# Kernel tuning notes

Measured on AMD Instinct MI355X. Metric: run time of the kernel, lower is better.

The kernel has to match this reference:

```python
import jax, jax.numpy as jnp
import numpy as np

N_GROUP = 8
TOPK_GROUP = 4
TOP_K = 8
ROUTED_SCALE = 2.5


def setup_inputs() -> dict:
    key = jax.random.key(0)
    ks = jax.random.split(key, 8)
    B, S, D, E, I = 4, 2048, 2048, 32, 1024
    s = 0.02
    return {
        "x": jax.random.normal(ks[0], (B, S, D), jnp.float32),
        "gate_w": jax.random.normal(ks[1], (D, E), jnp.float32) * s,
        "e_bias": jnp.zeros((E,), jnp.float32),
        "gate_up": jax.random.normal(ks[2], (E, D, 2 * I), jnp.float32) * s,
        "down": jax.random.normal(ks[3], (E, I, D), jnp.float32) * s,
        "shared_gate": jax.random.normal(ks[4], (D, I), jnp.float32) * s,
        "shared_up": jax.random.normal(ks[5], (D, I), jnp.float32) * s,
        "shared_down": jax.random.normal(ks[6], (I, D), jnp.float32) * s,
    }


def _router(x_flat, gate_w, e_bias):
    N, E = x_flat.shape[0], gate_w.shape[1]
    epg = E // N_GROUP  # experts per group
    logits = x_flat @ gate_w                                   # [N, E]
    scores = jax.nn.sigmoid(logits.astype(jnp.float32))        # [N, E]
    sfr = scores + e_bias                                      # routing scores
    grouped = sfr.reshape(N, N_GROUP, epg)
    group_scores = jax.lax.top_k(grouped, min(2, epg))[0].sum(-1)   # [N, G]
    topk_group_idx = jax.lax.top_k(group_scores, TOPK_GROUP)[1]     # [N, topk_group]
    group_mask = jnp.zeros((N, N_GROUP), bool).at[
        jnp.arange(N)[:, None], topk_group_idx].set(True)
    expert_mask = jnp.repeat(group_mask, epg, axis=1)          # [N, E]
    masked = jnp.where(expert_mask, sfr, -jnp.inf)
    topk_idx = jax.lax.top_k(masked, TOP_K)[1]                 # [N, K]
    topk_w = jnp.take_along_axis(scores, topk_idx, axis=1)     # [N, K]
    topk_w = topk_w / (topk_w.sum(-1, keepdims=True) + 1e-20)  # norm_topk_prob
    topk_w = topk_w * ROUTED_SCALE
    return topk_idx, topk_w, scores


def _experts(x_flat, topk_idx, topk_w, gate_up, down):
    N, D = x_flat.shape
    E, K = gate_up.shape[0], topk_idx.shape[1]
    flat = topk_idx.reshape(-1)                                # [N*K]
    sort_idx = jnp.argsort(flat)                               # route: group rows by expert
    sorted_tokens = x_flat[sort_idx // K]                      # [N*K, D]
    group_sizes = jnp.bincount(flat, length=E).astype(jnp.int32)
    h = jax.lax.ragged_dot(sorted_tokens, gate_up, group_sizes)  # [N*K, 2I]
    gate_h, up_h = jnp.split(h, 2, axis=-1)
    inter = jax.nn.silu(gate_h) * up_h                         # SwiGLU
    out = jax.lax.ragged_dot(inter, down, group_sizes)         # [N*K, D]
    unsorted = jnp.zeros_like(out).at[sort_idx].set(out)       # unroute
    return (unsorted.reshape(N, K, D) * topk_w[..., None].astype(out.dtype)).sum(1)


def _shared_mlp(x, wg, wu, wd):
    return (jax.nn.silu(x @ wg) * (x @ wu)) @ wd


def reference(x, gate_w, e_bias, gate_up, down, shared_gate, shared_up, shared_down):
    B, S, D = x.shape
    x_flat = x.reshape(B * S, D)
    topk_idx, topk_w, scores = _router(x_flat, gate_w, e_bias)
    routed = _experts(x_flat, topk_idx, topk_w, gate_up, down).reshape(B, S, D)
    output = routed + _shared_mlp(x, shared_gate, shared_up, shared_down)
    return output, topk_idx, scores
```

## Files before the change

### kernel.cpp

```cpp
#include <hip/hip_runtime.h>
#include <hip/hip_bf16.h>
#include <math.h>


typedef __bf16 bf16_t;
typedef __bf16 bf16x8 __attribute__((ext_vector_type(8)));
typedef float  f32x4  __attribute__((ext_vector_type(4)));

constexpr int NTOK = 8192;
constexpr int D    = 2048;
constexpr int E    = 32;
constexpr int I    = 1024;
constexpr int TK   = 8;
constexpr int NK   = NTOK * TK;
constexpr int TM   = 256;
constexpr int MAX_TILES = E + NK / TM;
constexpr float RSCALE = 2.5f;

#define GL16(g, l) __builtin_amdgcn_global_load_lds( \
    (const __attribute__((address_space(1))) void*)(g), \
    (__attribute__((address_space(3))) void*)(l), 16, 0, 0)


__global__ __launch_bounds__(64) void k_zero_meta(int* counts, int* cursors, int* ntl) {
    int t = threadIdx.x;
    if (t < E) { counts[t] = 0; cursors[t] = 0; }
    if (t == 0) *ntl = 0;
}

__global__ __launch_bounds__(64) void k_sentinel(float* out) {
    if (threadIdx.x == 0) out[0] = 12345.0f;
}

__global__ __launch_bounds__(256) void k_convert_x(const float* __restrict__ src,
                                                   bf16_t* __restrict__ dst, int n8) {
    int i = blockIdx.x * 256 + threadIdx.x;
    if (i >= n8) return;
    const float4* s = (const float4*)src;
    float4 a = s[(size_t)i * 2], b = s[(size_t)i * 2 + 1];
    bf16_t t[8] = {(bf16_t)a.x, (bf16_t)a.y, (bf16_t)a.z, (bf16_t)a.w,
                   (bf16_t)b.x, (bf16_t)b.y, (bf16_t)b.z, (bf16_t)b.w};
    *(uint4*)(dst + (size_t)i * 8) = *(const uint4*)t;
}

template <int MODE>
__global__ __launch_bounds__(256) void k_transpose(const float* __restrict__ src,
                                                   bf16_t* __restrict__ dst,
                                                   int R, int C,
                                                   size_t srcMat, size_t dstMat) {
    __shared__ float t[32][33];
    int b = blockIdx.z;
    const float* s = src + (size_t)b * srcMat;
    bf16_t* d = dst + (size_t)b * dstMat;
    int c0 = blockIdx.x * 32, r0 = blockIdx.y * 32;
    int tx = threadIdx.x, ty = threadIdx.y;
#pragma unroll
    for (int yy = 0; yy < 4; yy++)
        t[ty + yy * 8][tx] = s[(size_t)(r0 + ty + yy * 8) * C + c0 + tx];
    __syncthreads();
#pragma unroll
    for (int yy = 0; yy < 4; yy++) {
        int c = c0 + ty + yy * 8;
        int rc = (MODE == 0) ? c
               : (MODE == 1) ? ((c < I) ? 2 * c : 2 * (c - I) + 1)
               : (MODE == 2) ? 2 * c : 2 * c + 1;
        d[(size_t)rc * R + r0 + tx] = (bf16_t)t[tx][ty + yy * 8];
    }
}


__global__ __launch_bounds__(256) void k_router(const float* __restrict__ x,
                                                const float* __restrict__ gw,
                                                const float* __restrict__ eb,
                                                float* __restrict__ out_idx,
                                                float* __restrict__ out_scores,
                                                float* __restrict__ topk_w,
                                                int* __restrict__ tok_expert,
                                                int* __restrict__ counts) {
    int t = blockIdx.x;
    int tid = threadIdx.x;
    int e = tid & 31, part = tid >> 5;
    const float* xr = x + (size_t)t * D;
    float partial = 0.f;
    int d0 = part * 256;
    for (int d = d0; d < d0 + 256; d++)
        partial += xr[d] * gw[(size_t)d * E + e];

    __shared__ float red[8][32];
    __shared__ float sc[32], sfr[32];
    red[part][e] = partial;
    __syncthreads();
    if (tid < 32) {
        float l = 0.f;
#pragma unroll
        for (int p = 0; p < 8; p++) l += red[p][tid];
        float s = 1.f / (1.f + expf(-l));
        sc[tid] = s;
        sfr[tid] = s + eb[tid];
        out_scores[(size_t)t * E + tid] = s;
    }
    __syncthreads();
    if (tid == 0) {
        float gs[8];
#pragma unroll
        for (int g = 0; g < 8; g++) {
            float m1 = -1e30f, m2 = -1e30f;
#pragma unroll
            for (int i = 0; i < 4; i++) {
                float v = sfr[g * 4 + i];
                if (v > m1) { m2 = m1; m1 = v; } else if (v > m2) m2 = v;
            }
            gs[g] = m1 + m2;
        }
        bool gsel[8] = {false, false, false, false, false, false, false, false};
        for (int it = 0; it < 4; it++) {
            int bi = -1; float bv = -1e30f;
            for (int g = 0; g < 8; g++)
                if (!gsel[g] && gs[g] > bv) { bv = gs[g]; bi = g; }
            gsel[bi] = true;
        }
        float masked[32];
        for (int i = 0; i < 32; i++) masked[i] = gsel[i >> 2] ? sfr[i] : -1e30f;
        int idx[TK]; float w[TK]; float wsum = 0.f;
        for (int k = 0; k < TK; k++) {
            int bi = 0; float bv = -1e30f;
            for (int i = 0; i < 32; i++)
                if (masked[i] > bv) { bv = masked[i]; bi = i; }
            masked[bi] = -1e30f;
            idx[k] = bi; w[k] = sc[bi]; wsum += w[k];
        }
        float inv = RSCALE / (wsum + 1e-20f);
        for (int k = 0; k < TK; k++) {
            out_idx[(size_t)t * TK + k] = (float)idx[k];
            topk_w[(size_t)t * TK + k] = w[k] * inv;
            tok_expert[(size_t)t * TK + k] = idx[k];
            atomicAdd(&counts[idx[k]], 1);
        }
    }
}

__global__ __launch_bounds__(64) void k_offsets(const int* __restrict__ counts,
                                                int* __restrict__ offs,
                                                int4* __restrict__ ttbl,
                                                int* __restrict__ ntl) {
    if (threadIdx.x != 0) return;
    int off = 0, nt = 0;
    for (int e = 0; e < E; e++) {
        offs[e] = off;
        int c = counts[e];
        for (int r = 0; r < c; r += TM) {
            ttbl[nt] = make_int4(off + r, min(TM, c - r), e, 0);
            nt++;
        }
        off += c;
    }
    offs[E] = off;
    *ntl = nt;
}

__global__ __launch_bounds__(256) void k_scatter(const int* __restrict__ tok_expert,
                                                 const int* __restrict__ offs,
                                                 int* __restrict__ cursors,
                                                 int* __restrict__ slot_token,
                                                 int* __restrict__ slot_inv) {
    int i = blockIdx.x * 256 + threadIdx.x;
    if (i >= NK) return;
    int e = tok_expert[i];
    int pos = offs[e] + atomicAdd(&cursors[e], 1);
    slot_token[pos] = i >> 3;
    slot_inv[i] = pos;
}


#define SCB() __builtin_amdgcn_sched_barrier(0)
#define SG(m, n) __builtin_amdgcn_sched_group_barrier(m, n, 0)
#define SG_PLAIN() do { SG(0x30, 2); SG(0x8, 16); } while (0)
#define SG_PRE()   do { SG(0x100, 4); SG(0x30, 2); SG(0x8, 16); } while (0)
#define SG_RF()    do { SG(0x30, 2); SG(0x8, 4); SG(0x100, 2); SG(0x8, 4); \
    SG(0x100, 2); SG(0x8, 4); SG(0x100, 2); SG(0x8, 4); SG(0x100, 2); } while (0)
#define SG_PRERF() do { SG(0x100, 4); SG(0x30, 2); SG(0x8, 4); SG(0x100, 2); \
    SG(0x8, 4); SG(0x100, 2); SG(0x8, 4); SG(0x100, 2); SG(0x8, 4); SG(0x100, 2); } while (0)

#define PEND() do { asm volatile("s_waitcnt vmcnt(4)" ::: "memory"); \
    __builtin_amdgcn_s_barrier(); SCB(); } while (0)

#define SA2(b, rnd, k0) do { \
    GL16(gA[0][rnd] + (k0), smb + (b) * 65536 + (rnd) * 8192 + w * 1024); \
    GL16(gA[1][rnd] + (k0), smb + (b) * 65536 + 16384 + (rnd) * 8192 + w * 1024); } while (0)

#define SB(b, h, k0) do { \
    GL16(gB[h][0] + (k0), smb + (b) * 65536 + 32768 + (h) * 16384 + w * 1024); \
    GL16(gB[h][1] + (k0), smb + (b) * 65536 + 32768 + (h) * 16384 + 8192 + w * 1024); } while (0)

#define LDA(b, mh) do { _Pragma("unroll") for (int m_ = 0; m_ < 4; m_++) { \
    aF[m_][0] = *(const bf16x8*)(smb + (b) * 65536 + wm * 16384 + (mh) * 8192 + m_ * 2048 + lofs0); \
    aF[m_][1] = *(const bf16x8*)(smb + (b) * 65536 + wm * 16384 + (mh) * 8192 + m_ * 2048 + lofs1); } } while (0)

#define LDB(dst, b, nh) do { _Pragma("unroll") for (int n_ = 0; n_ < 2; n_++) { \
    dst[n_][0] = *(const bf16x8*)(smb + (b) * 65536 + 32768 + wn * 8192 + (nh) * 4096 + n_ * 2048 + lofs0); \
    dst[n_][1] = *(const bf16x8*)(smb + (b) * 65536 + 32768 + wn * 8192 + (nh) * 4096 + n_ * 2048 + lofs1); } } while (0)

#define MMA(bv, MH, NH) do { \
    __builtin_amdgcn_s_setprio(1); \
    _Pragma("unroll") for (int m_ = 0; m_ < 4; m_++) \
    _Pragma("unroll") for (int n_ = 0; n_ < 2; n_++) { \
    acc[(MH) * 4 + m_][(NH) * 2 + n_] = __builtin_amdgcn_mfma_f32_16x16x32_bf16( \
        aF[m_][0], bv[n_][0], acc[(MH) * 4 + m_][(NH) * 2 + n_], 0, 0, 0); \
    acc[(MH) * 4 + m_][(NH) * 2 + n_] = __builtin_amdgcn_mfma_f32_16x16x32_bf16( \
        aF[m_][1], bv[n_][1], acc[(MH) * 4 + m_][(NH) * 2 + n_], 0, 0, 0); } \
    __builtin_amdgcn_s_setprio(0); } while (0)

#define MMARF(bv, MH, NH, rb, rmh) do { \
    __builtin_amdgcn_s_setprio(1); \
    _Pragma("unroll") for (int m_ = 0; m_ < 4; m_++) { \
    _Pragma("unroll") for (int n_ = 0; n_ < 2; n_++) { \
    acc[(MH) * 4 + m_][(NH) * 2 + n_] = __builtin_amdgcn_mfma_f32_16x16x32_bf16( \
        aF[m_][0], bv[n_][0], acc[(MH) * 4 + m_][(NH) * 2 + n_], 0, 0, 0); \
    acc[(MH) * 4 + m_][(NH) * 2 + n_] = __builtin_amdgcn_mfma_f32_16x16x32_bf16( \
        aF[m_][1], bv[n_][1], acc[(MH) * 4 + m_][(NH) * 2 + n_], 0, 0, 0); } \
    aF[m_][0] = *(const bf16x8*)(smb + (rb) * 65536 + wm * 16384 + (rmh) * 8192 + m_ * 2048 + lofs0); \
    aF[m_][1] = *(const bf16x8*)(smb + (rb) * 65536 + wm * 16384 + (rmh) * 8192 + m_ * 2048 + lofs1); } \
    __builtin_amdgcn_s_setprio(0); } while (0)

template <bool EXPERT, bool GATHER, int EPI>
__global__ __launch_bounds__(512, 2) void k_mm8(const bf16_t* __restrict__ A,
                                                const bf16_t* __restrict__ Bt,
                                                int K, size_t estride,
                                                const int* __restrict__ slot_token,
                                                const int4* __restrict__ ttbl,
                                                const int* __restrict__ ntl,
                                                void* __restrict__ C, int ldc) {
    int L = (int)blockIdx.y * 8 + (int)blockIdx.x;
    int xcd = L & 7, k = L >> 3;
    int per = (int)gridDim.y >> 3;
    int ty = xcd * per + (k >> 3);
    int tx = k & 7;

    int base_slot, rows, e;
    if (EXPERT) {
        if (ty >= *ntl) return;
        int4 tt = ttbl[ty];
        base_slot = tt.x; rows = tt.y; e = tt.z;
    } else {
        base_slot = ty * TM; rows = TM; e = 0;
    }
    int c0 = tx * 256;
    const bf16_t* Bw = Bt + (size_t)e * estride + (size_t)c0 * K;

    extern __shared__ char smb[];

    int tid = threadIdx.x, lane = tid & 63, w = tid >> 6;
    int wm = w >> 2, wn = w & 3;
    int lr = lane & 15, hi = lane >> 4;
    int rx = lr & 7;
    int lofs0 = lr * 128 + ((hi ^ rx) << 4);
    int lofs1 = lr * 128 + (((4 + hi) ^ rx) << 4);

    int srow = tid >> 3;
    int cbg = (tid & 7) ^ (srow & 7);
    const bf16_t* gA[2][2]; const bf16_t* gB[2][2];
#pragma unroll
    for (int h = 0; h < 2; h++)
#pragma unroll
        for (int rnd = 0; rnd < 2; rnd++) {
            int r = h * 128 + rnd * 64 + srow;
            int ar = min(r, rows - 1);
            int tok = GATHER ? slot_token[base_slot + ar] : (base_slot + ar);
            gA[h][rnd] = A + (size_t)tok * K + cbg * 8;
            gB[h][rnd] = Bw + (size_t)r * K + cbg * 8;
        }

    f32x4 acc[8][4] = {};
    bf16x8 aF[4][2], b0[2][2], b1[2][2];

    SA2(0, 0, 0); SA2(0, 1, 0);
    SB(0, 0, 0); SB(0, 1, 0);
    SA2(1, 0, 64);
    SB(1, 0, 64); SB(1, 1, 64);
    asm volatile("s_waitcnt vmcnt(0)" ::: "memory");
    __builtin_amdgcn_s_barrier();
    SCB();
    LDA(0, 0); LDB(b0, 0, 0);

    int nt = K >> 6;
    for (int kt = 0; kt < nt; kt += 2) {
        int k1 = (kt + 1) << 6;
        int k2 = (kt + 2 < nt) ? (kt + 2) << 6 : 0;
        int k3 = (kt + 3 < nt) ? (kt + 3) << 6 : 0;
        LDB(b1, 0, 1);
        SA2(1, 1, k1);
        MMA(b0, 0, 0);
        SG_PRE(); PEND();
        SA2(0, 0, k2);
        MMARF(b1, 0, 1, 0, 1);
        SG_RF(); PEND();
        SB(0, 0, k2);
        MMA(b0, 1, 0);
        SG_PLAIN(); PEND();
        LDB(b0, 1, 0);
        SB(0, 1, k2);
        MMARF(b1, 1, 1, 1, 0);
        SG_PRERF(); PEND();
        LDB(b1, 1, 1);
        SA2(0, 1, k2);
        MMA(b0, 0, 0);
        SG_PRE(); PEND();
        SA2(1, 0, k3);
        MMARF(b1, 0, 1, 1, 1);
        SG_RF(); PEND();
        SB(1, 0, k3);
        MMA(b0, 1, 0);
        SG_PLAIN(); PEND();
        LDB(b0, 0, 0);
        SB(1, 1, k3);
        MMARF(b1, 1, 1, 0, 0);
        SG_PRERF(); PEND();
    }

#pragma unroll
    for (int mi = 0; mi < 8; mi++) {
#pragma unroll
        for (int j = 0; j < 4; j++) {
            int r = wm * 128 + mi * 16 + hi * 4 + j;
            bool valid = !EXPERT || (r < rows);
            size_t orow = (size_t)base_slot + r;
#pragma unroll
            for (int f = 0; f < 4; f++) {
                float v = acc[mi][f][j];
                int c = c0 + wn * 64 + f * 16 + lr;
                if (EPI == 0) {
                    float o = __shfl_xor(v, 1);
                    float g = (lane & 1) ? o : v;
                    float u = (lane & 1) ? v : o;
                    float sv = g / (1.f + __expf(-g)) * u;
                    if (valid && !(lane & 1))
                        ((bf16_t*)C)[orow * ldc + (c >> 1)] = (bf16_t)sv;
                } else if (EPI == 1) {
                    float o = __shfl_xor(v, 1);
                    if (valid && !(lane & 1)) {
                        bf16_t pr[2] = {(bf16_t)v, (bf16_t)o};
                        *(unsigned int*)((bf16_t*)C + orow * ldc + c) = *(unsigned int*)pr;
                    }
                } else {
                    if (valid) ((float*)C)[orow * ldc + c] = v;
                }
            }
        }
    }
}


__global__ __launch_bounds__(256) void k_finalize(const bf16_t* __restrict__ outS,
                                                  const int* __restrict__ slot_inv,
                                                  const float* __restrict__ tkw,
                                                  float* __restrict__ out) {
    int tok = blockIdx.x, tid = threadIdx.x;
    __shared__ int sp[TK];
    __shared__ float swt[TK];
    if (tid < TK) {
        sp[tid] = slot_inv[tok * TK + tid];
        swt[tid] = tkw[tok * TK + tid];
    }
    __syncthreads();
    int c = tid * 8;
    float* op = out + (size_t)tok * D + c;
    float acc[8];
    float4 o0 = *(float4*)op, o1 = *(float4*)(op + 4);
    acc[0] = o0.x; acc[1] = o0.y; acc[2] = o0.z; acc[3] = o0.w;
    acc[4] = o1.x; acc[5] = o1.y; acc[6] = o1.z; acc[7] = o1.w;
#pragma unroll
    for (int k = 0; k < TK; k++) {
        bf16x8 v = *(const bf16x8*)(outS + (size_t)sp[k] * D + c);
        float w = swt[k];
#pragma unroll
        for (int j = 0; j < 8; j++) acc[j] += w * (float)v[j];
    }
    o0 = make_float4(acc[0], acc[1], acc[2], acc[3]);
    o1 = make_float4(acc[4], acc[5], acc[6], acc[7]);
    *(float4*)op = o0;
    *(float4*)(op + 4) = o1;
}


extern "C" void kernel_launch(void* const* d_in, const int* in_sizes, int n_in,
                              void* d_out, int out_size, void* d_ws, size_t ws_size,
                              hipStream_t stream) {
    const float* x  = (const float*)d_in[0];
    const float* gw = (const float*)d_in[1];
    const float* eb = (const float*)d_in[2];
    const float* gu = (const float*)d_in[3];
    const float* dn = (const float*)d_in[4];
    const float* sg = (const float*)d_in[5];
    const float* su = (const float*)d_in[6];
    const float* sd = (const float*)d_in[7];

    float* out        = (float*)d_out;
    float* out_idx    = out + (size_t)NTOK * D;
    float* out_scores = out_idx + (size_t)NTOK * TK;

    char* w = (char*)d_ws;
    auto alloc = [&](size_t bytes) {
        char* p = w;
        w += (bytes + 255) & ~(size_t)255;
        return p;
    };
    bf16_t* xb      = (bf16_t*)alloc((size_t)NTOK * D * 2);
    bf16_t* gut     = (bf16_t*)alloc((size_t)E * 2 * I * D * 2);
    bf16_t* dnt     = (bf16_t*)alloc((size_t)E * D * I * 2);
    bf16_t* sh1t    = (bf16_t*)alloc((size_t)2 * I * D * 2);
    bf16_t* sdt     = (bf16_t*)alloc((size_t)D * I * 2);
    bf16_t* inter   = (bf16_t*)alloc((size_t)NK * I * 2);
    bf16_t* inter_s = (bf16_t*)alloc((size_t)NTOK * I * 2);
    float*  tkw     = (float*)alloc((size_t)NK * 4);
    int*    tke     = (int*)alloc((size_t)NK * 4);
    int*    stok    = (int*)alloc((size_t)NK * 4);
    int*    sinv    = (int*)alloc((size_t)NK * 4);
    int*    counts  = (int*)alloc(E * 4);
    int*    offs    = (int*)alloc((E + 1) * 4);
    int*    curs    = (int*)alloc(E * 4);
    int4*   ttbl    = (int4*)alloc(MAX_TILES * 16);
    int*    ntl     = (int*)alloc(4);
    bf16_t* outS    = gut;

    if ((size_t)(w - (char*)d_ws) > ws_size) {
        k_sentinel<<<1, 64, 0, stream>>>(out);
        return;
    }

    k_zero_meta<<<1, 64, 0, stream>>>(counts, curs, ntl);
    k_convert_x<<<(NTOK * D / 8 + 255) / 256, 256, 0, stream>>>(x, xb, NTOK * D / 8);

    k_transpose<1><<<dim3(2 * I / 32, D / 32, E), dim3(32, 8), 0, stream>>>(
        gu, gut, D, 2 * I, (size_t)D * 2 * I, (size_t)D * 2 * I);
    k_transpose<0><<<dim3(D / 32, I / 32, E), dim3(32, 8), 0, stream>>>(
        dn, dnt, I, D, (size_t)I * D, (size_t)I * D);
    k_transpose<2><<<dim3(I / 32, D / 32, 1), dim3(32, 8), 0, stream>>>(
        sg, sh1t, D, I, 0, 0);
    k_transpose<3><<<dim3(I / 32, D / 32, 1), dim3(32, 8), 0, stream>>>(
        su, sh1t, D, I, 0, 0);
    k_transpose<0><<<dim3(D / 32, I / 32, 1), dim3(32, 8), 0, stream>>>(
        sd, sdt, I, D, 0, 0);

    k_router<<<NTOK, 256, 0, stream>>>(x, gw, eb, out_idx, out_scores, tkw, tke, counts);
    k_offsets<<<1, 64, 0, stream>>>(counts, offs, ttbl, ntl);
    k_scatter<<<NK / 256, 256, 0, stream>>>(tke, offs, curs, stok, sinv);

    constexpr size_t SMEM = 131072;
    k_mm8<true, true, 0><<<dim3(8, MAX_TILES), 512, SMEM, stream>>>(
        xb, gut, D, (size_t)2 * I * D, stok, ttbl, ntl, inter, I);
    k_mm8<true, false, 1><<<dim3(8, MAX_TILES), 512, SMEM, stream>>>(
        inter, dnt, I, (size_t)D * I, stok, ttbl, ntl, outS, D);

    k_mm8<false, false, 0><<<dim3(8, NTOK / TM), 512, SMEM, stream>>>(
        xb, sh1t, D, 0, nullptr, nullptr, nullptr, inter_s, I);
    k_mm8<false, false, 2><<<dim3(8, NTOK / TM), 512, SMEM, stream>>>(
        inter_s, sdt, I, 0, nullptr, nullptr, nullptr, out, D);

    k_finalize<<<NTOK, 256, 0, stream>>>(outS, sinv, tkw, out);
}
```

Before: 1.809 ms.

## Merge shared-expert GEMMs into routed grouped GEMM launches and fuse x conversion into router

Shared-MLP row tiles are appended to the routed tile table, so one grouped-GEMM launch per stage handles both routed and shared work. This removes two launches and the tail where the shared GEMMs ran alone. The x-to-bf16 conversion moves into the router kernel, and the weight transposes switch to 64x64 tiles with float4 loads and 16-byte bf16 stores. In exchange the GEMM kernel picks pointers and epilogue per tile at runtime, which adds branches and register pressure. The grid also grows, which changes how the XCD tile remapping spreads work.

New measurement: 1.815 ms. Within noise of the previous version (+0.3%).

```diff
diff --git a/kernel.cpp b/kernel.cpp
--- a/kernel.cpp
+++ b/kernel.cpp
@@ -14,7 +14,8 @@
 constexpr int TK   = 8;
 constexpr int NK   = NTOK * TK;
 constexpr int TM   = 256;
-constexpr int MAX_TILES = E + NK / TM;
+constexpr int MAX_TILES  = E + NK / TM;
+constexpr int MAX_TILES2 = MAX_TILES + NTOK/TM;
 constexpr float RSCALE = 2.5f;
 
 #define GL16(g, l) __builtin_amdgcn_global_load_lds( \
@@ -32,39 +33,36 @@
     if (threadIdx.x == 0) out[0] = 12345.0f;
 }
 
-__global__ __launch_bounds__(256) void k_convert_x(const float* __restrict__ src,
-                                                   bf16_t* __restrict__ dst, int n8) {
-    int i = blockIdx.x * 256 + threadIdx.x;
-    if (i >= n8) return;
-    const float4* s = (const float4*)src;
-    float4 a = s[(size_t)i * 2], b = s[(size_t)i * 2 + 1];
-    bf16_t t[8] = {(bf16_t)a.x, (bf16_t)a.y, (bf16_t)a.z, (bf16_t)a.w,
-                   (bf16_t)b.x, (bf16_t)b.y, (bf16_t)b.z, (bf16_t)b.w};
-    *(uint4*)(dst + (size_t)i * 8) = *(const uint4*)t;
-}
-
 template <int MODE>
-__global__ __launch_bounds__(256) void k_transpose(const float* __restrict__ src,
-                                                   bf16_t* __restrict__ dst,
-                                                   int R, int C,
-                                                   size_t srcMat, size_t dstMat) {
-    __shared__ float t[32][33];
+__global__ __launch_bounds__(256) void k_transpose64(const float* __restrict__ src,
+                                                     bf16_t* __restrict__ dst,
+                                                     int R, int C,
+                                                     size_t srcMat, size_t dstMat) {
+    __shared__ float t[64][65];
     int b = blockIdx.z;
     const float* s = src + (size_t)b * srcMat;
     bf16_t* d = dst + (size_t)b * dstMat;
-    int c0 = blockIdx.x * 32, r0 = blockIdx.y * 32;
-    int tx = threadIdx.x, ty = threadIdx.y;
-#pragma unroll
-    for (int yy = 0; yy < 4; yy++)
-        t[ty + yy * 8][tx] = s[(size_t)(r0 + ty + yy * 8) * C + c0 + tx];
+    int c0 = blockIdx.x * 64, r0 = blockIdx.y * 64;
+    int tid = threadIdx.x;
+    int rr = tid >> 4, c4 = (tid & 15) * 4;
+#pragma unroll
+    for (int yy = 0; yy < 4; yy++) {
+        int r = yy * 16 + rr;
+        float4 v = *(const float4*)(s + (size_t)(r0 + r) * C + c0 + c4);
+        t[r][c4] = v.x; t[r][c4 + 1] = v.y; t[r][c4 + 2] = v.z; t[r][c4 + 3] = v.w;
+    }
     __syncthreads();
-#pragma unroll
-    for (int yy = 0; yy < 4; yy++) {
-        int c = c0 + ty + yy * 8;
+    int j = tid & 7, ccb = tid >> 3;
+#pragma unroll
+    for (int zz = 0; zz < 2; zz++) {
+        int c = c0 + zz * 32 + ccb;
         int rc = (MODE == 0) ? c
                : (MODE == 1) ? ((c < I) ? 2 * c : 2 * (c - I) + 1)
                : (MODE == 2) ? 2 * c : 2 * c + 1;
-        d[(size_t)rc * R + r0 + tx] = (bf16_t)t[tx][ty + yy * 8];
+        bf16_t tmp[8];
+#pragma unroll
+        for (int i = 0; i < 8; i++) tmp[i] = (bf16_t)t[j * 8 + i][zz * 32 + ccb];
+        *(uint4*)(d + (size_t)rc * R + r0 + j * 8) = *(const uint4*)tmp;
     }
 }
 
@@ -72,6 +70,7 @@
 __global__ __launch_bounds__(256) void k_router(const float* __restrict__ x,
                                                 const float* __restrict__ gw,
                                                 const float* __restrict__ eb,
+                                                bf16_t* __restrict__ xb,
                                                 float* __restrict__ out_idx,
                                                 float* __restrict__ out_scores,
                                                 float* __restrict__ topk_w,
@@ -79,8 +78,17 @@
                                                 int* __restrict__ counts) {
     int t = blockIdx.x;
     int tid = threadIdx.x;
+    const float* xr = x + (size_t)t * D;
+
+    {
+        int c = tid * 8;
+        float4 a = *(const float4*)(xr + c), b2 = *(const float4*)(xr + c + 4);
+        bf16_t tmp[8] = {(bf16_t)a.x, (bf16_t)a.y, (bf16_t)a.z, (bf16_t)a.w,
+                         (bf16_t)b2.x, (bf16_t)b2.y, (bf16_t)b2.z, (bf16_t)b2.w};
+        *(uint4*)(xb + (size_t)t * D + c) = *(const uint4*)tmp;
+    }
+
     int e = tid & 31, part = tid >> 5;
-    const float* xr = x + (size_t)t * D;
     float partial = 0.f;
     int d0 = part * 256;
     for (int d = d0; d < d0 + 256; d++)
@@ -155,6 +163,10 @@
         off += c;
     }
     offs[E] = off;
+    for (int i = 0; i < NTOK / TM; i++) {
+        ttbl[nt] = make_int4(i * TM, TM, 0, 1);
+        nt++;
+    }
     *ntl = nt;
 }
 
@@ -222,30 +234,31 @@
     aF[m_][1] = *(const bf16x8*)(smb + (rb) * 65536 + wm * 16384 + (rmh) * 8192 + m_ * 2048 + lofs1); } \
     __builtin_amdgcn_s_setprio(0); } while (0)
 
-template <bool EXPERT, bool GATHER, int EPI>
-__global__ __launch_bounds__(512, 2) void k_mm8(const bf16_t* __restrict__ A,
-                                                const bf16_t* __restrict__ Bt,
+template <int GEMM>
+__global__ __launch_bounds__(512, 2) void k_mm8(const bf16_t* __restrict__ Ae,
+                                                const bf16_t* __restrict__ Ash,
+                                                const bf16_t* __restrict__ Be,
+                                                const bf16_t* __restrict__ Bs,
                                                 int K, size_t estride,
                                                 const int* __restrict__ slot_token,
                                                 const int4* __restrict__ ttbl,
                                                 const int* __restrict__ ntl,
-                                                void* __restrict__ C, int ldc) {
+                                                void* __restrict__ Ce,
+                                                void* __restrict__ Cs, int ldc) {
     int L = (int)blockIdx.y * 8 + (int)blockIdx.x;
     int xcd = L & 7, k = L >> 3;
     int per = (int)gridDim.y >> 3;
     int ty = xcd * per + (k >> 3);
     int tx = k & 7;
 
-    int base_slot, rows, e;
-    if (EXPERT) {
-        if (ty >= *ntl) return;
-        int4 tt = ttbl[ty];
-        base_slot = tt.x; rows = tt.y; e = tt.z;
-    } else {
-        base_slot = ty * TM; rows = TM; e = 0;
-    }
+    if (ty >= *ntl) return;
+    int4 tt = ttbl[ty];
+    int base_slot = tt.x, rows = tt.y, e = tt.z, flag = tt.w;
+    const bf16_t* A = flag ? Ash : Ae;
+    bool gather = (GEMM == 1) && !flag;
+
     int c0 = tx * 256;
-    const bf16_t* Bw = Bt + (size_t)e * estride + (size_t)c0 * K;
+    const bf16_t* Bw = (flag ? Bs : Be + (size_t)e * estride) + (size_t)c0 * K;
 
     extern __shared__ char smb[];
 
@@ -265,7 +278,7 @@
         for (int rnd = 0; rnd < 2; rnd++) {
             int r = h * 128 + rnd * 64 + srow;
             int ar = min(r, rows - 1);
-            int tok = GATHER ? slot_token[base_slot + ar] : (base_slot + ar);
+            int tok = gather ? slot_token[base_slot + ar] : (base_slot + ar);
             gA[h][rnd] = A + (size_t)tok * K + cbg * 8;
             gB[h][rnd] = Bw + (size_t)r * K + cbg * 8;
         }
@@ -322,27 +335,30 @@
 #pragma unroll
         for (int j = 0; j < 4; j++) {
             int r = wm * 128 + mi * 16 + hi * 4 + j;
-            bool valid = !EXPERT || (r < rows);
+            bool valid = (r < rows);
             size_t orow = (size_t)base_slot + r;
 #pragma unroll
             for (int f = 0; f < 4; f++) {
                 float v = acc[mi][f][j];
                 int c = c0 + wn * 64 + f * 16 + lr;
-                if (EPI == 0) {
+                if (GEMM == 1) {
                     float o = __shfl_xor(v, 1);
                     float g = (lane & 1) ? o : v;
                     float u = (lane & 1) ? v : o;
                     float sv = g / (1.f + __expf(-g)) * u;
+                    bf16_t* Cp = (bf16_t*)(flag ? Cs : Ce);
                     if (valid && !(lane & 1))
-                        ((bf16_t*)C)[orow * ldc + (c >> 1)] = (bf16_t)sv;
-                } else if (EPI == 1) {
-                    float o = __shfl_xor(v, 1);
-                    if (valid && !(lane & 1)) {
-                        bf16_t pr[2] = {(bf16_t)v, (bf16_t)o};
-                        *(unsigned int*)((bf16_t*)C + orow * ldc + c) = *(unsigned int*)pr;
+                        Cp[orow * ldc + (c >> 1)] = (bf16_t)sv;
+                } else {
+                    if (flag) {
+                        if (valid) ((float*)Cs)[orow * ldc + c] = v;
+                    } else {
+                        float o = __shfl_xor(v, 1);
+                        if (valid && !(lane & 1)) {
+                            bf16_t pr[2] = {(bf16_t)v, (bf16_t)o};
+                            *(unsigned int*)((bf16_t*)Ce + orow * ldc + c) = *(unsigned int*)pr;
+                        }
                     }
-                } else {
-                    if (valid) ((float*)C)[orow * ldc + c] = v;
                 }
             }
         }
@@ -418,7 +434,7 @@
     int*    counts  = (int*)alloc(E * 4);
     int*    offs    = (int*)alloc((E + 1) * 4);
     int*    curs    = (int*)alloc(E * 4);
-    int4*   ttbl    = (int4*)alloc(MAX_TILES * 16);
+    int4*   ttbl    = (int4*)alloc(MAX_TILES2 * 16);
     int*    ntl     = (int*)alloc(4);
     bf16_t* outS    = gut;
 
@@ -428,33 +444,27 @@
     }
 
     k_zero_meta<<<1, 64, 0, stream>>>(counts, curs, ntl);
-    k_convert_x<<<(NTOK * D / 8 + 255) / 256, 256, 0, stream>>>(x, xb, NTOK * D / 8);
-
-    k_transpose<1><<<dim3(2 * I / 32, D / 32, E), dim3(32, 8), 0, stream>>>(
+
+    k_transpose64<1><<<dim3(2 * I / 64, D / 64, E), 256, 0, stream>>>(
         gu, gut, D, 2 * I, (size_t)D * 2 * I, (size_t)D * 2 * I);
-    k_transpose<0><<<dim3(D / 32, I / 32, E), dim3(32, 8), 0, stream>>>(
+    k_transpose64<0><<<dim3(D / 64, I / 64, E), 256, 0, stream>>>(
         dn, dnt, I, D, (size_t)I * D, (size_t)I * D);
-    k_transpose<2><<<dim3(I / 32, D / 32, 1), dim3(32, 8), 0, stream>>>(
+    k_transpose64<2><<<dim3(I / 64, D / 64, 1), 256, 0, stream>>>(
         sg, sh1t, D, I, 0, 0);
-    k_transpose<3><<<dim3(I / 32, D / 32, 1), dim3(32, 8), 0, stream>>>(
+    k_transpose64<3><<<dim3(I / 64, D / 64, 1), 256, 0, stream>>>(
         su, sh1t, D, I, 0, 0);
-    k_transpose<0><<<dim3(D / 32, I / 32, 1), dim3(32, 8), 0, stream>>>(
+    k_transpose64<0><<<dim3(D / 64, I / 64, 1), 256, 0, stream>>>(
         sd, sdt, I, D, 0, 0);
 
-    k_router<<<NTOK, 256, 0, stream>>>(x, gw, eb, out_idx, out_scores, tkw, tke, counts);
+    k_router<<<NTOK, 256, 0, stream>>>(x, gw, eb, xb, out_idx, out_scores, tkw, tke, counts);
     k_offsets<<<1, 64, 0, stream>>>(counts, offs, ttbl, ntl);
     k_scatter<<<NK / 256, 256, 0, stream>>>(tke, offs, curs, stok, sinv);
 
     constexpr size_t SMEM = 131072;
-    k_mm8<true, true, 0><<<dim3(8, MAX_TILES), 512, SMEM, stream>>>(
-        xb, gut, D, (size_t)2 * I * D, stok, ttbl, ntl, inter, I);
-    k_mm8<true, false, 1><<<dim3(8, MAX_TILES), 512, SMEM, stream>>>(
-        inter, dnt, I, (size_t)D * I, stok, ttbl, ntl, outS, D);
-
-    k_mm8<false, false, 0><<<dim3(8, NTOK / TM), 512, SMEM, stream>>>(
-        xb, sh1t, D, 0, nullptr, nullptr, nullptr, inter_s, I);
-    k_mm8<false, false, 2><<<dim3(8, NTOK / TM), 512, SMEM, stream>>>(
-        inter_s, sdt, I, 0, nullptr, nullptr, nullptr, out, D);
+    k_mm8<1><<<dim3(8, MAX_TILES2), 512, SMEM, stream>>>(
+        xb, xb, gut, sh1t, D, (size_t)2 * I * D, stok, ttbl, ntl, inter, inter_s, I);
+    k_mm8<2><<<dim3(8, MAX_TILES2), 512, SMEM, stream>>>(
+        inter, inter_s, dnt, sdt, I, (size_t)D * I, stok, ttbl, ntl, outS, out, D);
 
     k_finalize<<<NTOK, 256, 0, stream>>>(outS, sinv, tkw, out);
 }
```
